# Optimization experiments

Hardware: AMD Instinct MI355X
Metric: run time of the kernel (lower is better)

## Reference

```python
import jax, jax.numpy as jnp
import numpy as np

TEMPLATE0 = 3  # template[0]: prefix prompt length, positions [t0, t0+count) are kept verbatim

def setup_inputs() -> dict:
    key = jax.random.key(0)
    ks = jax.random.split(key, 6)
    B, S, H, E = 16, 512, 768, 19
    scale = 1.0 / np.sqrt(H)
    return {
        "sequence_output": jax.random.normal(ks[0], (B, S, H), jnp.float32),
        "label_init": jax.random.normal(ks[1], (E, H), jnp.float32),
        "attn_w": jax.random.normal(ks[2], (H, H), jnp.float32) * scale,
        "attn_b": jax.random.normal(ks[3], (H,), jnp.float32) * scale,
        "fc_w": jax.random.normal(ks[4], (H,), jnp.float32) * scale,
        "counts": jax.random.randint(ks[5], (B,), 1, 400, jnp.int32),
    }

def reference(sequence_output, label_init, attn_w, attn_b, fc_w, counts):
    # Vectorized form of GPT2SoftmaxForNer_LE.add_label_embedding + attention
    B, S, H = sequence_output.shape
    # attn_linear: torch Linear -> x @ W^T + b
    x_attn = jnp.einsum('bsh,gh->bsg', sequence_output, attn_w) + attn_b  # [B,S,H]
    # att_features = label_embedding + expanded input state; e = tanh(...)
    e = jnp.tanh(x_attn[:, :, None, :] + label_init[None, None, :, :])  # [B,S,E,H]
    scores = jnp.einsum('bseh,h->bse', e, fc_w)  # fc: Linear(H,1,bias=False)
    attn_dist = jax.nn.softmax(scores, axis=-1)
    # (original renormalizes softmax by its sum; sum==1 so it is a no-op)
    ctx = jnp.einsum('bse,eh->bsh', attn_dist, label_init)
    out = ctx + sequence_output  # residual add
    # restore original embeddings at positions [t0, t0 + counts[b])
    pos = jnp.arange(S)[None, :]  # [1,S]
    keep = (pos >= TEMPLATE0) & (pos < counts[:, None] + TEMPLATE0)  # [B,S]
    return jnp.where(keep[:, :, None], sequence_output, out)
```

## Files before the change

### kernel.cpp

```cpp
#include <hip/hip_runtime.h>
#include <hip/hip_fp16.h>

typedef __bf16 bf16_t;
typedef __bf16 bf16x8 __attribute__((ext_vector_type(8)));
typedef _Float16 f16_t;
typedef _Float16 f16x2 __attribute__((ext_vector_type(2)));
typedef _Float16 f16x8 __attribute__((ext_vector_type(8)));
typedef float  f32x4  __attribute__((ext_vector_type(4)));

#define B_ 16
#define S_ 512
#define H_ 768
#define E_ 19
#define T0 3
#define ROWS (B_*S_)
#define SCAL 2.8853900817779268f
#define ECLAMP_LO (-13.5f)
#define ECLAMP_HI (15.5f)

#define WS_W_OFF  0
#define WS_W_SZ   (H_*H_*2)
#define WS_PL_OFF (WS_W_OFF + WS_W_SZ)
#define WS_PL_SZ  (E_*H_*2)
#define WS_FC_OFF (WS_PL_OFF + WS_PL_SZ)
#define WS_FC_SZ  (H_*2)
#define WS_PX_OFF (WS_FC_OFF + WS_FC_SZ)
#define WS_PX_SZ  (ROWS*H_*2)
#define WS_NEED   (WS_PX_OFF + WS_PX_SZ)
#define WS_AB_OFF WS_NEED
#define WS_AB_SZ  (ROWS*H_*2)
#define WS_NEED2  (WS_AB_OFF + WS_AB_SZ)

__device__ __forceinline__ f16_t h_rcp(f16_t x) {
  __half hx = __builtin_bit_cast(__half, x);
  return __builtin_bit_cast(f16_t, hrcp(hx));
}
__device__ __forceinline__ float clamp_e(float v) {
  return fminf(fmaxf(v, ECLAMP_LO), ECLAMP_HI);
}

__global__ __launch_bounds__(256) void prep_kernel(
    const float* __restrict__ w, const float* __restrict__ lab,
    const float* __restrict__ attb, const float* __restrict__ fcw,
    const float* __restrict__ seq,
    bf16_t* __restrict__ wbf, f16_t* __restrict__ pls,
    f16_t* __restrict__ fcg, bf16_t* __restrict__ abf) {
  int t = blockIdx.x*256 + threadIdx.x;
  int i = t*8;
  if (i < H_*H_) {
    float4 u = *(const float4*)(w + i);
    float4 v = *(const float4*)(w + i + 4);
    bf16x8 b;
    b[0]=(bf16_t)(u.x*SCAL); b[1]=(bf16_t)(u.y*SCAL); b[2]=(bf16_t)(u.z*SCAL); b[3]=(bf16_t)(u.w*SCAL);
    b[4]=(bf16_t)(v.x*SCAL); b[5]=(bf16_t)(v.y*SCAL); b[6]=(bf16_t)(v.z*SCAL); b[7]=(bf16_t)(v.w*SCAL);
    *(bf16x8*)(wbf + i) = b;
  }
  if (t < E_*H_) {
    int col = t % H_;
    float e2 = clamp_e((lab[t] + attb[col]) * SCAL);
    pls[t] = (f16_t)__builtin_amdgcn_exp2f(e2);
  }
  if (t < H_) fcg[t] = (f16_t)fcw[t];
  if (i < ROWS*H_) {
    float4 u = *(const float4*)(seq + i);
    float4 v = *(const float4*)(seq + i + 4);
    bf16x8 b;
    b[0]=(bf16_t)u.x; b[1]=(bf16_t)u.y; b[2]=(bf16_t)u.z; b[3]=(bf16_t)u.w;
    b[4]=(bf16_t)v.x; b[5]=(bf16_t)v.y; b[6]=(bf16_t)v.z; b[7]=(bf16_t)v.w;
    *(bf16x8*)(abf + i) = b;
  }
}

#define G_BM 128
#define G_BN 128
#define G_BK 64
#define G_NT 256
#define G_STEPS (H_/G_BK)

__global__ __launch_bounds__(G_NT, 2) void gemm_xs2(
    const bf16_t* __restrict__ abf,
    const bf16_t* __restrict__ wbf, f16_t* __restrict__ px) {
  __shared__ __align__(16) unsigned char smem[32768];
  const int tid  = threadIdx.x;
  const int lane = tid & 63, wv = tid >> 6;
  const int bid  = blockIdx.x;
  const int wg   = (bid & 7)*48 + (bid >> 3);
  const int rt   = wg / 6, ct = wg % 6;
  const int arow0 = rt * G_BM;
  const int bcol0 = ct * G_BN;
  const int wr = wv >> 1, wc = wv & 1;
  const int ar = lane & 15, kg = lane >> 4;

  f32x4 acc[4][4] = {};

  auto stage = [&](int s) {
    const int k0 = s * G_BK;
    #pragma unroll
    for (int it = 0; it < 4; ++it) {
      int Lb  = (wv*4 + it) * 1024;
      int L   = Lb + lane*16;
      int row = L >> 7;
      int c   = (L >> 4) & 7;
      int cs  = c ^ (row & 7);
      const bf16_t* srcA = abf + (size_t)(arow0 + row)*H_ + k0 + cs*8;
      __builtin_amdgcn_global_load_lds(
          (const __attribute__((address_space(1))) void*)srcA,
          (__attribute__((address_space(3))) void*)(smem + Lb), 16, 0, 0);
      const bf16_t* srcB = wbf + (size_t)(bcol0 + row)*H_ + k0 + cs*8;
      __builtin_amdgcn_global_load_lds(
          (const __attribute__((address_space(1))) void*)srcB,
          (__attribute__((address_space(3))) void*)(smem + 16384 + Lb), 16, 0, 0);
    }
  };

  stage(0);
  #pragma unroll 1
  for (int s = 0; s < G_STEPS; ++s) {
    __syncthreads();
    #pragma unroll
    for (int ks = 0; ks < 2; ++ks) {
      bf16x8 af[4], bfr[4];
      #pragma unroll
      for (int mf = 0; mf < 4; ++mf) {
        int row = wr*64 + mf*16 + ar;
        int g2  = ks*4 + kg;
        af[mf] = *(const bf16x8*)(smem + row*128 + ((g2 ^ (row & 7)) << 4));
      }
      #pragma unroll
      for (int nf = 0; nf < 4; ++nf) {
        int row = wc*64 + nf*16 + ar;
        int g2  = ks*4 + kg;
        bfr[nf] = *(const bf16x8*)(smem + 16384 + row*128 + ((g2 ^ (row & 7)) << 4));
      }
      #pragma unroll
      for (int mf = 0; mf < 4; ++mf)
        #pragma unroll
        for (int nf = 0; nf < 4; ++nf)
          acc[mf][nf] = __builtin_amdgcn_mfma_f32_16x16x32_bf16(af[mf], bfr[nf], acc[mf][nf], 0,0,0);
    }
    __syncthreads();
    if (s + 1 < G_STEPS) stage(s + 1);
  }

  #pragma unroll
  for (int mf = 0; mf < 4; ++mf) {
    int rbase = arow0 + wr*64 + mf*16 + kg*4;
    #pragma unroll
    for (int nf = 0; nf < 4; ++nf) {
      int col = bcol0 + wc*64 + nf*16 + ar;
      #pragma unroll
      for (int i = 0; i < 4; ++i) {
        float v = clamp_e(acc[mf][nf][i]);
        px[(size_t)(rbase + i)*H_ + col] = (f16_t)__builtin_amdgcn_exp2f(v);
      }
    }
  }
}

#define K2_R   4
#define K2_PAD 1552
#define K2_SALL (K2_R*K2_PAD)
#define K2_PP   (K2_SALL + K2_R*20*4)
#define K2_LDS  (K2_PP + K2_R*20*4)
__global__ __launch_bounds__(256, 6) void score_ctx(
    const f16_t* __restrict__ px, const f16_t* __restrict__ pls,
    const f16_t* __restrict__ fcg, const float* __restrict__ seq,
    const float* __restrict__ lab, const int* __restrict__ counts,
    float* __restrict__ out) {
  __shared__ __align__(16) unsigned char smem[K2_LDS];
  float* Sall = (float*)(smem + K2_SALL);
  float* Pp   = (float*)(smem + K2_PP);
  const int tid = threadIdx.x;
  const int r0  = blockIdx.x * K2_R;

  for (int i = tid; i < K2_R*(H_/8); i += 256) {
    int row = i / 96, kv = i % 96;
    f16x8 v = *(const f16x8*)(px + (size_t)(r0 + row)*H_ + kv*8);
    *(f16x8*)(smem + row*K2_PAD + kv*16) = v;
  }
  __syncthreads();

  const int g = tid >> 4, k = tid & 15;
  const int r = g & 3, eq = g >> 2;
  const f16_t* xrow = (const f16_t*)(smem + r*K2_PAD + k*96);
  const int ebase = eq*5;
  const f16_t* lbase = pls + ebase*H_ + k*48;
  const f16_t one = (f16_t)1.0f;
  const f16x8 one8 = {one,one,one,one,one,one,one,one};

  float s[5] = {};
  #pragma unroll 1
  for (int c = 0; c < 6; ++c) {
    f16x8 xh  = *(const f16x8*)(xrow + c*8);
    f16x8 fch = *(const f16x8*)(fcg + k*48 + c*8);
    #pragma unroll
    for (int j = 0; j < 5; ++j) {
      if (j == 4 && eq == 3) continue;
      f16x8 lh = *(const f16x8*)(lbase + j*H_ + c*8);
      f16x8 u  = xh*lh + one8;
      f16x8 rr;
      #pragma unroll
      for (int q = 0; q < 8; ++q) rr[q] = h_rcp(u[q]);
      const f16x2* rp = (const f16x2*)&rr;
      const f16x2* fp = (const f16x2*)&fch;
      #pragma unroll
      for (int p = 0; p < 4; ++p)
        s[j] = __builtin_amdgcn_fdot2(rp[p], fp[p], s[j], false);
    }
  }
  #pragma unroll
  for (int off = 1; off < 16; off <<= 1)
    #pragma unroll
    for (int j = 0; j < 5; ++j)
      s[j] += __shfl_xor(s[j], off, 64);
  if (k == 0) {
    #pragma unroll
    for (int j = 0; j < 5; ++j) {
      int e = ebase + j;
      if (e < E_) Sall[r*20 + e] = s[j];
    }
  }
  __syncthreads();

  if (tid < K2_R) {
    float s2[E_]; float mx = -1e30f;
    #pragma unroll
    for (int e = 0; e < E_; ++e) {
      float v = -2.0f * Sall[tid*20 + e];
      s2[e] = v; mx = fmaxf(mx, v);
    }
    float ssum = 0.f;
    #pragma unroll
    for (int e = 0; e < E_; ++e) {
      float pr = __builtin_amdgcn_exp2f((s2[e] - mx) * 1.4426950408889634f);
      s2[e] = pr; ssum += pr;
    }
    float rr = __builtin_amdgcn_rcpf(ssum);
    #pragma unroll
    for (int e = 0; e < E_; ++e) Pp[tid*20 + e] = s2[e]*rr;
  }
  __syncthreads();

  if (tid < 192) {
    f32x4 o4[K2_R] = {};
    #pragma unroll 1
    for (int e = 0; e < E_; ++e) {
      f32x4 la = *(const f32x4*)(lab + e*H_ + tid*4);
      #pragma unroll
      for (int rr2 = 0; rr2 < K2_R; ++rr2) {
        float pv = Pp[rr2*20 + e];
        o4[rr2] += pv * la;
      }
    }
    const int batch = r0 >> 9;
    const int cnt = counts[batch];
    #pragma unroll
    for (int rr2 = 0; rr2 < K2_R; ++rr2) {
      int row = r0 + rr2;
      int sp  = row & 511;
      bool keep = (sp >= T0) && (sp < cnt + T0);
      size_t idx = (size_t)row*H_ + tid*4;
      f32x4 sv = *(const f32x4*)(seq + idx);
      f32x4 ov = keep ? sv : (sv + o4[rr2]);
      *(f32x4*)(out + idx) = ov;
    }
  }
}

#define BM 16
#define NW 6
#define NT (NW*64)
#define A_SZ   (BM*H_*2)
#define LS_OFF A_SZ
#define LS_SZ  (E_*H_*2)
#define LDS_SZ (A_SZ + LS_SZ)
#define SP_OFF 0
#define PP_OFF (NW*BM*20*4)

__global__ __launch_bounds__(NT, 3) void ner_fused(
    const float* __restrict__ seq, const float* __restrict__ lab,
    const float* __restrict__ attw, const float* __restrict__ attb,
    const float* __restrict__ fcw, const int* __restrict__ counts,
    float* __restrict__ out)
{
  __shared__ __align__(16) unsigned char smem[LDS_SZ];
  _Float16* Lsh = (_Float16*)(smem + LS_OFF);
  float* Sp = (float*)(smem + SP_OFF);
  float* Pp = (float*)(smem + PP_OFF);
  const int tid   = threadIdx.x;
  const int blk   = blockIdx.x;
  const int batch = blk >> 5;
  const int s0    = (blk & 31) * BM;
  const size_t rowbase = ((size_t)batch * S_ + s0) * H_;
  {
    const float4* src = (const float4*)(seq + rowbase);
    #pragma unroll
    for (int i = 0; i < (BM*H_/8)/NT; ++i) {
      int idx = i*NT + tid;
      int row = idx / (H_/8);
      int kv  = idx % (H_/8);
      float4 u = src[row*(H_/4) + kv*2];
      float4 v = src[row*(H_/4) + kv*2 + 1];
      bf16x8 b;
      b[0]=(bf16_t)u.x; b[1]=(bf16_t)u.y; b[2]=(bf16_t)u.z; b[3]=(bf16_t)u.w;
      b[4]=(bf16_t)v.x; b[5]=(bf16_t)v.y; b[6]=(bf16_t)v.z; b[7]=(bf16_t)v.w;
      int byte = row*(H_*2) + kv*16;
      *(bf16x8*)(smem + (byte ^ ((row & 7) << 4))) = b;
    }
  }
  for (int i = tid*4; i < E_*H_; i += NT*4) {
    int c = i % H_;
    float4 l4 = *(const float4*)(lab + i);
    float4 b4 = *(const float4*)(attb + c);
    int e = i / H_;
    #pragma unroll
    for (int j = 0; j < 4; ++j) {
      int col = c + j;
      int wv2 = col >> 7, rr = col & 127, n = rr >> 4, arr = rr & 15;
      float v = ((&l4.x)[j] + (&b4.x)[j]) * SCAL;
      Lsh[((e*NW + wv2)*16 + arr)*8 + n] = (_Float16)v;
    }
  }
  __syncthreads();
  const int lane = tid & 63;
  const int wv   = tid >> 6;
  const int ar   = lane & 15;
  const int kg   = lane >> 4;
  const int wbase = wv * (H_/NW);
  f32x4 acc[8] = {};
  {
    const int a_sw = (ar & 7) << 4;
    #pragma unroll 1
    for (int step = 0; step < H_/32; ++step) {
      int kb = step*64 + kg*16;
      bf16x8 a0 = *(const bf16x8*)(smem + ((ar*1536 + kb) ^ a_sw));
      int k = step*32 + kg*8;
      #pragma unroll
      for (int n = 0; n < 8; ++n) {
        int gcol = wbase + n*16 + ar;
        float4 u = *(const float4*)(attw + (size_t)gcol*H_ + k);
        float4 v = *(const float4*)(attw + (size_t)gcol*H_ + k + 4);
        bf16x8 bb;
        bb[0]=(bf16_t)(u.x*SCAL); bb[1]=(bf16_t)(u.y*SCAL); bb[2]=(bf16_t)(u.z*SCAL); bb[3]=(bf16_t)(u.w*SCAL);
        bb[4]=(bf16_t)(v.x*SCAL); bb[5]=(bf16_t)(v.y*SCAL); bb[6]=(bf16_t)(v.z*SCAL); bb[7]=(bf16_t)(v.w*SCAL);
        acc[n] = __builtin_amdgcn_mfma_f32_16x16x32_bf16(a0, bb, acc[n], 0,0,0);
      }
    }
  }
  __syncthreads();
  float fcv[8];
  #pragma unroll
  for (int n = 0; n < 8; ++n) fcv[n] = fcw[wbase + n*16 + ar];
  {
    const _Float16* Lw = Lsh + (wv*16 + ar)*8;
    #pragma unroll 1
    for (int e = 0; e < E_; ++e) {
      f16x8 lh = *(const f16x8*)(Lw + e*(NW*128));
      float lv[8];
      #pragma unroll
      for (int n = 0; n < 8; ++n) lv[n] = (float)lh[n];
      float s8[4] = {};
      #pragma unroll
      for (int n = 0; n < 8; ++n)
        #pragma unroll
        for (int i = 0; i < 4; ++i) {
          float t = __builtin_amdgcn_exp2f(acc[n][i] + lv[n]);
          s8[i] += fcv[n] * __builtin_amdgcn_rcpf(t + 1.0f);
        }
      #pragma unroll
      for (int off = 1; off < 16; off <<= 1)
        #pragma unroll
        for (int i = 0; i < 4; ++i)
          s8[i] += __shfl_xor(s8[i], off, 64);
      if (ar == 0) {
        #pragma unroll
        for (int i = 0; i < 4; ++i)
          Sp[(wv*BM + kg*4 + i)*20 + e] = s8[i];
      }
    }
  }
  __syncthreads();
  if (tid % 24 == 0) {
    int row = tid / 24;
    float sc2[E_];
    float mx = -1e30f;
    #pragma unroll
    for (int e = 0; e < E_; ++e) {
      float v = 0.f;
      #pragma unroll
      for (int w2 = 0; w2 < NW; ++w2) v += Sp[(w2*BM + row)*20 + e];
      sc2[e] = -2.0f * v;
      mx = fmaxf(mx, sc2[e]);
    }
    float ssum = 0.f;
    #pragma unroll
    for (int e = 0; e < E_; ++e) {
      float p = __builtin_amdgcn_exp2f((sc2[e] - mx) * 1.4426950408889634f);
      sc2[e] = p; ssum += p;
    }
    float rr = __builtin_amdgcn_rcpf(ssum);
    #pragma unroll
    for (int e = 0; e < E_; ++e) Pp[row*20 + e] = sc2[e]*rr;
  }
  __syncthreads();
  {
    const int cg = tid % 96;
    const int rq = tid / 96;
    float o[4][8] = {};
    const f32x4* L4 = (const f32x4*)lab;
    #pragma unroll 1
    for (int e = 0; e < E_; ++e) {
      f32x4 la = L4[e*(H_/4) + cg*2];
      f32x4 lb = L4[e*(H_/4) + cg*2 + 1];
      #pragma unroll
      for (int rr2 = 0; rr2 < 4; ++rr2) {
        float p = Pp[(rq*4 + rr2)*20 + e];
        o[rr2][0] += p*la[0]; o[rr2][1] += p*la[1]; o[rr2][2] += p*la[2]; o[rr2][3] += p*la[3];
        o[rr2][4] += p*lb[0]; o[rr2][5] += p*lb[1]; o[rr2][6] += p*lb[2]; o[rr2][7] += p*lb[3];
      }
    }
    const int cnt = counts[batch];
    #pragma unroll
    for (int rr2 = 0; rr2 < 4; ++rr2) {
      int row = rq*4 + rr2;
      int sp  = s0 + row;
      bool keep = (sp >= T0) && (sp < cnt + T0);
      size_t idx = rowbase + (size_t)row*H_ + cg*8;
      float4 s1 = *(const float4*)(seq + idx);
      float4 s2v = *(const float4*)(seq + idx + 4);
      float4 o1, o2;
      if (keep) { o1 = s1; o2 = s2v; }
      else {
        o1 = make_float4(s1.x + o[rr2][0], s1.y + o[rr2][1], s1.z + o[rr2][2], s1.w + o[rr2][3]);
        o2 = make_float4(s2v.x + o[rr2][4], s2v.y + o[rr2][5], s2v.z + o[rr2][6], s2v.w + o[rr2][7]);
      }
      *(float4*)(out + idx)     = o1;
      *(float4*)(out + idx + 4) = o2;
    }
  }
}

extern "C" void kernel_launch(void* const* d_in, const int* in_sizes, int n_in,
                              void* d_out, int out_size, void* d_ws, size_t ws_size,
                              hipStream_t stream) {
  const float* seq    = (const float*)d_in[0];
  const float* lab    = (const float*)d_in[1];
  const float* attw   = (const float*)d_in[2];
  const float* attb   = (const float*)d_in[3];
  const float* fcw    = (const float*)d_in[4];
  const int*   counts = (const int*)d_in[5];
  float* out = (float*)d_out;

  if (ws_size >= (size_t)WS_NEED) {
    bf16_t* wbf = (bf16_t*)((char*)d_ws + WS_W_OFF);
    f16_t*  pls = (f16_t*)((char*)d_ws + WS_PL_OFF);
    f16_t*  fcg = (f16_t*)((char*)d_ws + WS_FC_OFF);
    f16_t*  pxp = (f16_t*)((char*)d_ws + WS_PX_OFF);
    bf16_t* abf = (ws_size >= (size_t)WS_NEED2)
                ? (bf16_t*)((char*)d_ws + WS_AB_OFF)
                : (bf16_t*)d_out;
    prep_kernel<<<dim3((ROWS*H_/8 + 255)/256), dim3(256), 0, stream>>>(
        attw, lab, attb, fcw, seq, wbf, pls, fcg, abf);
    gemm_xs2<<<dim3((ROWS/G_BM)*(H_/G_BN)), dim3(G_NT), 0, stream>>>(
        abf, wbf, pxp);
    score_ctx<<<dim3(ROWS/K2_R), dim3(256), 0, stream>>>(
        pxp, pls, fcg, seq, lab, counts, out);
  } else {
    ner_fused<<<dim3(ROWS/BM), dim3(NT), 0, stream>>>(seq, lab, attw, attb, fcw, counts, out);
  }
}
```

Before: 60.18 us.

## Fuse fp32-to-bf16 activation conversion into GEMM tile loads

```diff
diff --git a/kernel.cpp b/kernel.cpp
--- a/kernel.cpp
+++ b/kernel.cpp
@@ -27,9 +27,6 @@
 #define WS_PX_OFF (WS_FC_OFF + WS_FC_SZ)
 #define WS_PX_SZ  (ROWS*H_*2)
 #define WS_NEED   (WS_PX_OFF + WS_PX_SZ)
-#define WS_AB_OFF WS_NEED
-#define WS_AB_SZ  (ROWS*H_*2)
-#define WS_NEED2  (WS_AB_OFF + WS_AB_SZ)
 
 __device__ __forceinline__ f16_t h_rcp(f16_t x) {
   __half hx = __builtin_bit_cast(__half, x);
@@ -42,9 +39,8 @@
 __global__ __launch_bounds__(256) void prep_kernel(
     const float* __restrict__ w, const float* __restrict__ lab,
     const float* __restrict__ attb, const float* __restrict__ fcw,
-    const float* __restrict__ seq,
     bf16_t* __restrict__ wbf, f16_t* __restrict__ pls,
-    f16_t* __restrict__ fcg, bf16_t* __restrict__ abf) {
+    f16_t* __restrict__ fcg) {
   int t = blockIdx.x*256 + threadIdx.x;
   int i = t*8;
   if (i < H_*H_) {
@@ -61,14 +57,6 @@
     pls[t] = (f16_t)__builtin_amdgcn_exp2f(e2);
   }
   if (t < H_) fcg[t] = (f16_t)fcw[t];
-  if (i < ROWS*H_) {
-    float4 u = *(const float4*)(seq + i);
-    float4 v = *(const float4*)(seq + i + 4);
-    bf16x8 b;
-    b[0]=(bf16_t)u.x; b[1]=(bf16_t)u.y; b[2]=(bf16_t)u.z; b[3]=(bf16_t)u.w;
-    b[4]=(bf16_t)v.x; b[5]=(bf16_t)v.y; b[6]=(bf16_t)v.z; b[7]=(bf16_t)v.w;
-    *(bf16x8*)(abf + i) = b;
-  }
 }
 
 #define G_BM 128
@@ -76,11 +64,12 @@
 #define G_BK 64
 #define G_NT 256
 #define G_STEPS (H_/G_BK)
+#define A_BYTES 32768
 
 __global__ __launch_bounds__(G_NT, 2) void gemm_xs2(
-    const bf16_t* __restrict__ abf,
+    const float* __restrict__ seq,
     const bf16_t* __restrict__ wbf, f16_t* __restrict__ px) {
-  __shared__ __align__(16) unsigned char smem[32768];
+  __shared__ __align__(16) unsigned char smem[49152];
   const int tid  = threadIdx.x;
   const int lane = tid & 63, wv = tid >> 6;
   const int bid  = blockIdx.x;
@@ -96,20 +85,28 @@
   auto stage = [&](int s) {
     const int k0 = s * G_BK;
     #pragma unroll
+    for (int it = 0; it < 8; ++it) {
+      int Lb  = (wv*8 + it) * 1024;
+      int L   = Lb + lane*16;
+      int row = L >> 8;
+      int c   = (L >> 4) & 15;
+      int cs  = c ^ (row & 7);
+      const float* srcA = seq + (size_t)(arow0 + row)*H_ + k0 + cs*4;
+      __builtin_amdgcn_global_load_lds(
+          (const __attribute__((address_space(1))) void*)srcA,
+          (__attribute__((address_space(3))) void*)(smem + Lb), 16, 0, 0);
+    }
+    #pragma unroll
     for (int it = 0; it < 4; ++it) {
       int Lb  = (wv*4 + it) * 1024;
       int L   = Lb + lane*16;
       int row = L >> 7;
       int c   = (L >> 4) & 7;
       int cs  = c ^ (row & 7);
-      const bf16_t* srcA = abf + (size_t)(arow0 + row)*H_ + k0 + cs*8;
-      __builtin_amdgcn_global_load_lds(
-          (const __attribute__((address_space(1))) void*)srcA,
-          (__attribute__((address_space(3))) void*)(smem + Lb), 16, 0, 0);
       const bf16_t* srcB = wbf + (size_t)(bcol0 + row)*H_ + k0 + cs*8;
       __builtin_amdgcn_global_load_lds(
           (const __attribute__((address_space(1))) void*)srcB,
-          (__attribute__((address_space(3))) void*)(smem + 16384 + Lb), 16, 0, 0);
+          (__attribute__((address_space(3))) void*)(smem + 32768 + Lb), 16, 0, 0);
     }
   };
 
@@ -123,14 +120,20 @@
       #pragma unroll
       for (int mf = 0; mf < 4; ++mf) {
         int row = wr*64 + mf*16 + ar;
+        int key = row & 7;
         int g2  = ks*4 + kg;
-        af[mf] = *(const bf16x8*)(smem + row*128 + ((g2 ^ (row & 7)) << 4));
+        f32x4 lo = *(const f32x4*)(smem + row*256 + (((2*g2)     ^ key) << 4));
+        f32x4 hi = *(const f32x4*)(smem + row*256 + (((2*g2 + 1) ^ key) << 4));
+        bf16x8 b;
+        b[0]=(bf16_t)lo[0]; b[1]=(bf16_t)lo[1]; b[2]=(bf16_t)lo[2]; b[3]=(bf16_t)lo[3];
+        b[4]=(bf16_t)hi[0]; b[5]=(bf16_t)hi[1]; b[6]=(bf16_t)hi[2]; b[7]=(bf16_t)hi[3];
+        af[mf] = b;
       }
       #pragma unroll
       for (int nf = 0; nf < 4; ++nf) {
         int row = wc*64 + nf*16 + ar;
         int g2  = ks*4 + kg;
-        bfr[nf] = *(const bf16x8*)(smem + 16384 + row*128 + ((g2 ^ (row & 7)) << 4));
+        bfr[nf] = *(const bf16x8*)(smem + 32768 + row*128 + ((g2 ^ (row & 7)) << 4));
       }
       #pragma unroll
       for (int mf = 0; mf < 4; ++mf)
@@ -456,13 +459,10 @@
     f16_t*  pls = (f16_t*)((char*)d_ws + WS_PL_OFF);
     f16_t*  fcg = (f16_t*)((char*)d_ws + WS_FC_OFF);
     f16_t*  pxp = (f16_t*)((char*)d_ws + WS_PX_OFF);
-    bf16_t* abf = (ws_size >= (size_t)WS_NEED2)
-                ? (bf16_t*)((char*)d_ws + WS_AB_OFF)
-                : (bf16_t*)d_out;
-    prep_kernel<<<dim3((ROWS*H_/8 + 255)/256), dim3(256), 0, stream>>>(
-        attw, lab, attb, fcw, seq, wbf, pls, fcg, abf);
+    prep_kernel<<<dim3((H_*H_/8 + 255)/256), dim3(256), 0, stream>>>(
+        attw, lab, attb, fcw, wbf, pls, fcg);
     gemm_xs2<<<dim3((ROWS/G_BM)*(H_/G_BN)), dim3(G_NT), 0, stream>>>(
-        abf, wbf, pxp);
+        seq, wbf, pxp);
     score_ctx<<<dim3(ROWS/K2_R), dim3(256), 0, stream>>>(
         pxp, pls, fcg, seq, lab, counts, out);
   } else {
```

Result: slower. 62.65 us (+4.1%).
